# Kernel optimization log

Measured on AMD Instinct MI355X. Metric: run time of the kernel, lower is better.

## Reference

```python
import jax, jax.numpy as jnp
import numpy as np

D_MODEL = 1024
HEADS = 16
D_FF = 2048
EPS = 1e-6


def _ln(z, alpha, beta):
    # Faithful to the repo's (buggy-looking) LayerNorm:
    # mu = z - mean; sigma = std + eps; out = (z - mu/sigma)*alpha + beta
    mean = jnp.mean(z, axis=-1, keepdims=True)
    std = jnp.std(z, axis=-1, keepdims=True, ddof=1)  # torch.std is unbiased
    return (z - (z - mean) / (std + EPS)) * alpha + beta


def setup_inputs() -> dict:
    key = jax.random.key(0)
    ks = jax.random.split(key, 16)
    B, S, D = 8, 1024, D_MODEL
    s = 0.02
    inp = {
        "x": jax.random.normal(ks[0], (B, S, D), dtype=jnp.float32),
        "mask": jax.random.randint(ks[1], (B, S), 0, 2, dtype=jnp.int32),
        "Wq": jax.random.normal(ks[2], (D, D), dtype=jnp.float32) * s,
        "bq": jnp.zeros((D,), dtype=jnp.float32),
        "Wk": jax.random.normal(ks[3], (D, D), dtype=jnp.float32) * s,
        "bk": jnp.zeros((D,), dtype=jnp.float32),
        "Wv": jax.random.normal(ks[4], (D, D), dtype=jnp.float32) * s,
        "bv": jnp.zeros((D,), dtype=jnp.float32),
        "Wo": jax.random.normal(ks[5], (D, D), dtype=jnp.float32) * s,
        "bo": jnp.zeros((D,), dtype=jnp.float32),
        "W1": jax.random.normal(ks[6], (D_FF, D), dtype=jnp.float32) * s,
        "b1": jnp.zeros((D_FF,), dtype=jnp.float32),
        "W2": jax.random.normal(ks[7], (D, D_FF), dtype=jnp.float32) * s,
        "b2": jnp.zeros((D,), dtype=jnp.float32),
        "alpha1": jnp.ones((D,), dtype=jnp.float32),
        "beta1": jnp.zeros((D,), dtype=jnp.float32),
        "alpha2": jnp.ones((D,), dtype=jnp.float32),
        "beta2": jnp.zeros((D,), dtype=jnp.float32),
    }
    return inp


def reference(x, mask, Wq, bq, Wk, bk, Wv, bv, Wo, bo, W1, b1, W2, b2,
              alpha1, beta1, alpha2, beta2):
    B, S, D = x.shape
    H, dk = HEADS, D // HEADS
    # QKV projections (torch Linear: y = x @ W.T + b), split heads -> [B,H,S,dk]
    Q = (x @ Wq.T + bq).reshape(B, S, H, dk).transpose(0, 2, 1, 3)
    K = (x @ Wk.T + bk).reshape(B, S, H, dk).transpose(0, 2, 1, 3)
    V = (x @ Wv.T + bv).reshape(B, S, H, dk).transpose(0, 2, 1, 3)
    scores = jnp.einsum('bhqd,bhkd->bhqk', Q, K) / jnp.sqrt(jnp.float32(dk))
    # faithful mask broadcast: [B,1,S,1] over query rows
    m = mask[:, None, :, None]
    scores = jnp.where(m == 0, jnp.float32(-1e9), scores)
    A = jax.nn.softmax(scores, axis=-1)
    O = jnp.einsum('bhqk,bhkd->bhqd', A, V).transpose(0, 2, 1, 3).reshape(B, S, D)
    attn_out = O @ Wo.T + bo
    x1 = _ln(x + attn_out, alpha1, beta1)
    h = jax.nn.relu(x1 @ W1.T + b1)
    ff = h @ W2.T + b2
    return _ln(x1 + ff, alpha2, beta2)
```

## Files before the change

### kernel.cpp

```cpp
#include <hip/hip_runtime.h>
#include <cstdint>
#include <cstddef>

#define D_MODEL 1024
#define HEADS   16
#define DKH     64
#define D_FF    2048
#define SEQ     1024
#define BATCH   8
#define MROWS   (BATCH*SEQ)
#define LN_EPS  1e-6f

typedef __bf16 bh8 __attribute__((ext_vector_type(8)));
typedef float  f32x4 __attribute__((ext_vector_type(4)));
typedef unsigned short us8 __attribute__((ext_vector_type(8)));

__device__ __forceinline__ unsigned short f2bf(float f) {
  union { float f; unsigned int u; } c; c.f = f;
  unsigned int u = c.u;
  u = u + 0x7fffu + ((u >> 16) & 1u);
  return (unsigned short)(u >> 16);
}

__device__ __forceinline__ bh8 as_bh8(us8 v) { return __builtin_bit_cast(bh8, v); }

__device__ __forceinline__ void gl16(const unsigned short* g, unsigned short* l) {
  __builtin_amdgcn_global_load_lds(
      (const __attribute__((address_space(1))) unsigned int*)g,
      (__attribute__((address_space(3))) unsigned int*)l, 16, 0, 0);
}

__global__ void cast_bf16_k(const float* __restrict__ in, unsigned short* __restrict__ out, int n4) {
  int i = blockIdx.x * blockDim.x + threadIdx.x;
  if (i < n4) {
    float4 v = ((const float4*)in)[i];
    ushort4 o;
    o.x = f2bf(v.x); o.y = f2bf(v.y); o.z = f2bf(v.z); o.w = f2bf(v.w);
    ((ushort4*)out)[i] = o;
  }
}

__global__ void castw_k(const float* __restrict__ wq, const float* __restrict__ wk,
                        const float* __restrict__ wv, const float* __restrict__ wo,
                        const float* __restrict__ w1, const float* __restrict__ w2,
                        unsigned short* __restrict__ oqkv, unsigned short* __restrict__ oo,
                        unsigned short* __restrict__ o1, unsigned short* __restrict__ o2) {
  int i = blockIdx.x * blockDim.x + threadIdx.x;
  const int seg = i >> 18;
  const int loc = i & 262143;
  const float* src; unsigned short* dst; int il, ol;
  if (seg < 3)      { src = (seg == 0) ? wq : (seg == 1) ? wk : wv; dst = oqkv; il = loc; ol = seg * 262144 + loc; }
  else if (seg == 3){ src = wo; dst = oo; il = loc; ol = loc; }
  else if (seg < 6) { src = w1; dst = o1; il = (seg - 4) * 262144 + loc; ol = il; }
  else              { src = w2; dst = o2; il = (seg - 6) * 262144 + loc; ol = il; }
  float4 v = ((const float4*)src)[il];
  ushort4 o;
  o.x = f2bf(v.x); o.y = f2bf(v.y); o.z = f2bf(v.z); o.w = f2bf(v.w);
  ((ushort4*)dst)[ol] = o;
}

#define BM 128
#define BN 128
#define BK 64

template<int EPI>
__global__ __launch_bounds__(256)
void gemm_bt(const unsigned short* __restrict__ A, const unsigned short* __restrict__ Bw,
             const float* __restrict__ b0, const float* __restrict__ b1f,
             const float* __restrict__ b2f, const float* __restrict__ resid,
             void* __restrict__ out0, void* __restrict__ out1, void* __restrict__ out2,
             int M, int N, int K)
{
  __shared__ __align__(16) unsigned short As[BM * BK];
  __shared__ __align__(16) unsigned short Bs[BN * BK];

  const int tid  = threadIdx.x;
  const int lane = tid & 63;
  const int w    = tid >> 6;
  const int wr   = w >> 1;
  const int wc   = w & 1;
  const int l15  = lane & 15;
  const int l4   = lane >> 4;

  const int brow = blockIdx.y * BM;
  const int bcol = blockIdx.x * BN;

  int rowj[4], offj[4];
  #pragma unroll
  for (int j = 0; j < 4; ++j) {
    const int c = tid + j * 256;
    rowj[j] = c >> 3;
    offj[j] = ((c & 7) ^ ((c >> 3) & 7)) * 8;
  }

  const unsigned short* Ag = A  + (size_t)brow * K;
  const unsigned short* Bg = Bw + (size_t)bcol * K;

  f32x4 acc[4][4] = {};
  const int sw7 = l15 & 7;

  for (int k0 = 0; k0 < K; k0 += BK) {
    #pragma unroll
    for (int j = 0; j < 4; ++j)
      gl16(Ag + (size_t)rowj[j] * K + k0 + offj[j], &As[(tid + j * 256) * 8]);
    #pragma unroll
    for (int j = 0; j < 4; ++j)
      gl16(Bg + (size_t)rowj[j] * K + k0 + offj[j], &Bs[(tid + j * 256) * 8]);
    __syncthreads();

    #pragma unroll
    for (int h = 0; h < 2; ++h) {
      const int slot = ((h * 4 + l4) ^ sw7) * 8;
      us8 aF[4], bF[4];
      #pragma unroll
      for (int mi = 0; mi < 4; ++mi)
        aF[mi] = *(const us8*)(&As[(wr * 64 + mi * 16 + l15) * BK + slot]);
      #pragma unroll
      for (int ni = 0; ni < 4; ++ni)
        bF[ni] = *(const us8*)(&Bs[(wc * 64 + ni * 16 + l15) * BK + slot]);
      #pragma unroll
      for (int mi = 0; mi < 4; ++mi)
        #pragma unroll
        for (int ni = 0; ni < 4; ++ni)
          acc[mi][ni] = __builtin_amdgcn_mfma_f32_16x16x32_bf16(
              as_bh8(aF[mi]), as_bh8(bF[ni]), acc[mi][ni], 0, 0, 0);
    }
    __syncthreads();
  }

  const int tt = bcol >> 10;
  #pragma unroll
  for (int mi = 0; mi < 4; ++mi) {
    #pragma unroll
    for (int ni = 0; ni < 4; ++ni) {
      const int gcol = bcol + wc * 64 + ni * 16 + l15;
      if (EPI == 4) {
        const int ccol = gcol & 1023;
        const float bv = ((tt == 0) ? b0 : (tt == 1) ? b1f : b2f)[ccol];
        const int grow0 = brow + wr * 64 + mi * 16 + l4 * 4;
        if (tt == 2) {
          const int bb = grow0 >> 10;
          const int s0 = grow0 & 1023;
          ushort4 pk;
          pk.x = f2bf(acc[mi][ni][0] + bv);
          pk.y = f2bf(acc[mi][ni][1] + bv);
          pk.z = f2bf(acc[mi][ni][2] + bv);
          pk.w = f2bf(acc[mi][ni][3] + bv);
          *(ushort4*)((unsigned short*)out2 + ((size_t)bb * D_MODEL + ccol) * SEQ + s0) = pk;
        } else {
          unsigned short* ob = (unsigned short*)(tt == 0 ? out0 : out1);
          #pragma unroll
          for (int v = 0; v < 4; ++v)
            ob[(size_t)(grow0 + v) * D_MODEL + ccol] = f2bf(acc[mi][ni][v] + bv);
        }
      } else {
        const float bv = b0[gcol];
        #pragma unroll
        for (int v = 0; v < 4; ++v) {
          const int grow = brow + wr * 64 + mi * 16 + l4 * 4 + v;
          float val = acc[mi][ni][v] + bv;
          if (EPI == 3) val = fmaxf(val, 0.0f);
          if (EPI == 2) {
            val += resid[(size_t)grow * N + gcol];
            ((float*)out0)[(size_t)grow * N + gcol] = val;
          } else {
            ((unsigned short*)out0)[(size_t)grow * N + gcol] = f2bf(val);
          }
        }
      }
    }
  }
}

__global__ __launch_bounds__(256)
void attn_k(const unsigned short* __restrict__ Q, const unsigned short* __restrict__ Kb,
            const unsigned short* __restrict__ Vt, const int* __restrict__ mask,
            unsigned short* __restrict__ O)
{
  __shared__ __align__(16) unsigned short Ks[2][64][64];
  __shared__ __align__(16) unsigned short Vs[2][64][64];
  __shared__ __align__(16) unsigned short Pl[4][16][88];

  const int bid = blockIdx.x;
  const int qc = bid & 15;
  const int h  = (bid >> 4) & 15;
  const int b  = bid >> 8;
  const int q0 = qc * 64;

  const int tid  = threadIdx.x;
  const int lane = tid & 63;
  const int w    = tid >> 6;
  const int l15  = lane & 15;
  const int l4   = lane >> 4;

  const int c0 = tid, c1 = tid + 256;
  const int kr0 = c0 >> 3, ke0 = ((c0 & 7) ^ (kr0 & 7)) * 8;
  const int kr1 = c1 >> 3, ke1 = ((c1 & 7) ^ (kr1 & 7)) * 8;

  const unsigned short* Kbase = Kb + ((size_t)b * SEQ) * D_MODEL + h * DKH;
  const unsigned short* Vbase = Vt + ((size_t)b * D_MODEL + h * DKH) * SEQ;

  const unsigned short* qp = Q + ((size_t)(b * SEQ + q0 + w * 16 + l15)) * D_MODEL + h * DKH + l4 * 8;
  const bh8 aQ0 = as_bh8(*(const us8*)qp);
  const bh8 aQ1 = as_bh8(*(const us8*)(qp + 32));

  float msel[4];
  #pragma unroll
  for (int v = 0; v < 4; ++v)
    msel[v] = mask[b * SEQ + q0 + w * 16 + l4 * 4 + v] ? 0.125f : 0.0f;

  float l[4] = {0.f, 0.f, 0.f, 0.f};
  f32x4 oacc[4] = {};

  gl16(Kbase + (size_t)kr0 * D_MODEL + ke0, &Ks[0][0][0] + c0 * 8);
  gl16(Kbase + (size_t)kr1 * D_MODEL + ke1, &Ks[0][0][0] + c1 * 8);
  gl16(Vbase + (size_t)kr0 * SEQ + ke0,     &Vs[0][0][0] + c0 * 8);
  gl16(Vbase + (size_t)kr1 * SEQ + ke1,     &Vs[0][0][0] + c1 * 8);
  __syncthreads();

  for (int t = 0; t < 16; ++t) {
    const int cur = t & 1;
    if (t < 15) {
      const int kv = (t + 1) * 64;
      gl16(Kbase + (size_t)(kv + kr0) * D_MODEL + ke0, &Ks[cur ^ 1][0][0] + c0 * 8);
      gl16(Kbase + (size_t)(kv + kr1) * D_MODEL + ke1, &Ks[cur ^ 1][0][0] + c1 * 8);
      gl16(Vbase + (size_t)kr0 * SEQ + kv + ke0,       &Vs[cur ^ 1][0][0] + c0 * 8);
      gl16(Vbase + (size_t)kr1 * SEQ + kv + ke1,       &Vs[cur ^ 1][0][0] + c1 * 8);
    }

    f32x4 s[4];
    #pragma unroll
    for (int kt = 0; kt < 4; ++kt) {
      const int row = kt * 16 + l15;
      const int swz = l15 & 7;
      bh8 bK0 = as_bh8(*(const us8*)(&Ks[cur][row][(l4 ^ swz) * 8]));
      bh8 bK1 = as_bh8(*(const us8*)(&Ks[cur][row][((4 + l4) ^ swz) * 8]));
      f32x4 t0 = {0.f, 0.f, 0.f, 0.f};
      t0 = __builtin_amdgcn_mfma_f32_16x16x32_bf16(aQ0, bK0, t0, 0, 0, 0);
      t0 = __builtin_amdgcn_mfma_f32_16x16x32_bf16(aQ1, bK1, t0, 0, 0, 0);
      s[kt] = t0;
    }

    #pragma unroll
    for (int v = 0; v < 4; ++v) {
      float ls = 0.f;
      #pragma unroll
      for (int kt = 0; kt < 4; ++kt) {
        float e = __expf(s[kt][v] * msel[v]);
        s[kt][v] = e;
        ls += e;
      }
      l[v] += ls;
    }

    #pragma unroll
    for (int kt = 0; kt < 4; ++kt)
      #pragma unroll
      for (int v = 0; v < 4; ++v)
        Pl[w][l4 * 4 + v][kt * 16 + l15] = f2bf(s[kt][v]);

    #pragma unroll
    for (int ks = 0; ks < 2; ++ks) {
      bh8 aP = as_bh8(*(const us8*)(&Pl[w][l15][ks * 32 + l4 * 8]));
      #pragma unroll
      for (int ds = 0; ds < 4; ++ds) {
        const int row = ds * 16 + l15;
        bh8 bV = as_bh8(*(const us8*)(&Vs[cur][row][((ks * 4 + l4) ^ (l15 & 7)) * 8]));
        oacc[ds] = __builtin_amdgcn_mfma_f32_16x16x32_bf16(aP, bV, oacc[ds], 0, 0, 0);
      }
    }
    __syncthreads();
  }

  #pragma unroll
  for (int v = 0; v < 4; ++v) {
    float lv = l[v];
    #pragma unroll
    for (int d = 1; d < 16; d <<= 1) lv += __shfl_xor(lv, d, 64);
    const float inv = 1.0f / lv;
    const int q = q0 + w * 16 + l4 * 4 + v;
    #pragma unroll
    for (int ds = 0; ds < 4; ++ds)
      O[((size_t)(b * SEQ + q)) * D_MODEL + h * DKH + ds * 16 + l15] =
          f2bf(oacc[ds][v] * inv);
  }
}

template<bool WBF>
__global__ __launch_bounds__(256)
void ln_k(const float* __restrict__ z, const float* __restrict__ alpha,
          const float* __restrict__ beta, float* __restrict__ yf,
          unsigned short* __restrict__ yb)
{
  const int row = blockIdx.x;
  const int tid = threadIdx.x;
  const float4 v = ((const float4*)(z + (size_t)row * D_MODEL))[tid];
  float s  = v.x + v.y + v.z + v.w;
  float ss = v.x * v.x + v.y * v.y + v.z * v.z + v.w * v.w;
  #pragma unroll
  for (int d = 1; d < 64; d <<= 1) {
    s  += __shfl_xor(s, d, 64);
    ss += __shfl_xor(ss, d, 64);
  }
  __shared__ float red[8];
  const int w = tid >> 6;
  if ((tid & 63) == 0) { red[w * 2] = s; red[w * 2 + 1] = ss; }
  __syncthreads();
  const float S  = red[0] + red[2] + red[4] + red[6];
  const float SS = red[1] + red[3] + red[5] + red[7];
  const float mean = S * (1.0f / 1024.0f);
  float var = (SS - 1024.0f * mean * mean) * (1.0f / 1023.0f);
  var = fmaxf(var, 0.0f);
  const float invd = 1.0f / (sqrtf(var) + LN_EPS);

  const float4 a  = ((const float4*)alpha)[tid];
  const float4 be = ((const float4*)beta)[tid];
  float4 y;
  y.x = (v.x - (v.x - mean) * invd) * a.x + be.x;
  y.y = (v.y - (v.y - mean) * invd) * a.y + be.y;
  y.z = (v.z - (v.z - mean) * invd) * a.z + be.z;
  y.w = (v.w - (v.w - mean) * invd) * a.w + be.w;
  ((float4*)(yf + (size_t)row * D_MODEL))[tid] = y;
  if (WBF) {
    ushort4 pk;
    pk.x = f2bf(y.x); pk.y = f2bf(y.y); pk.z = f2bf(y.z); pk.w = f2bf(y.w);
    ((ushort4*)(yb + (size_t)row * D_MODEL))[tid] = pk;
  }
}

extern "C" void kernel_launch(void* const* d_in, const int* in_sizes, int n_in,
                              void* d_out, int out_size, void* d_ws, size_t ws_size,
                              hipStream_t stream) {
  const float* x    = (const float*)d_in[0];
  const int*   mask = (const int*)d_in[1];
  const float* Wq = (const float*)d_in[2];  const float* bq = (const float*)d_in[3];
  const float* Wk = (const float*)d_in[4];  const float* bk = (const float*)d_in[5];
  const float* Wv = (const float*)d_in[6];  const float* bv = (const float*)d_in[7];
  const float* Wo = (const float*)d_in[8];  const float* bo = (const float*)d_in[9];
  const float* W1 = (const float*)d_in[10]; const float* b1 = (const float*)d_in[11];
  const float* W2 = (const float*)d_in[12]; const float* b2 = (const float*)d_in[13];
  const float* alpha1 = (const float*)d_in[14]; const float* beta1 = (const float*)d_in[15];
  const float* alpha2 = (const float*)d_in[16]; const float* beta2 = (const float*)d_in[17];
  (void)in_sizes; (void)n_in; (void)out_size; (void)ws_size;

  char* ws = (char*)d_ws;
  const size_t MB = (size_t)1 << 20;
  unsigned short* xb    = (unsigned short*)(ws + 0 * MB);
  unsigned short* Wqkvb = (unsigned short*)(ws + 16 * MB);
  unsigned short* Wob   = (unsigned short*)(ws + 22 * MB);
  unsigned short* W1b   = (unsigned short*)(ws + 24 * MB);
  unsigned short* W2b   = (unsigned short*)(ws + 28 * MB);
  unsigned short* Qb    = (unsigned short*)(ws + 32 * MB);
  unsigned short* Kb2   = (unsigned short*)(ws + 48 * MB);
  unsigned short* Vt    = (unsigned short*)(ws + 64 * MB);
  unsigned short* Ob    = (unsigned short*)(ws + 80 * MB);
  float*          zf    = (float*)(ws + 96 * MB);
  float*          x1f   = (float*)(ws + 128 * MB);
  unsigned short* x1b   = (unsigned short*)(ws + 160 * MB);
  unsigned short* hb    = Qb;

  cast_bf16_k<<<8192, 256, 0, stream>>>(x, xb, MROWS * D_MODEL / 4);
  castw_k<<<8192, 256, 0, stream>>>(Wq, Wk, Wv, Wo, W1, W2, Wqkvb, Wob, W1b, W2b);

  gemm_bt<4><<<dim3(24, 64), 256, 0, stream>>>(xb, Wqkvb, bq, bk, bv, nullptr,
                                               Qb, Kb2, Vt, MROWS, 3072, D_MODEL);

  attn_k<<<BATCH * HEADS * (SEQ / 64), 256, 0, stream>>>(Qb, Kb2, Vt, mask, Ob);

  gemm_bt<2><<<dim3(8, 64), 256, 0, stream>>>(Ob, Wob, bo, nullptr, nullptr, x,
                                              zf, nullptr, nullptr, MROWS, D_MODEL, D_MODEL);
  ln_k<true><<<MROWS, 256, 0, stream>>>(zf, alpha1, beta1, x1f, x1b);

  gemm_bt<3><<<dim3(16, 64), 256, 0, stream>>>(x1b, W1b, b1, nullptr, nullptr, nullptr,
                                               hb, nullptr, nullptr, MROWS, D_FF, D_MODEL);
  gemm_bt<2><<<dim3(8, 64), 256, 0, stream>>>(hb, W2b, b2, nullptr, nullptr, x1f,
                                              zf, nullptr, nullptr, MROWS, D_MODEL, D_FF);

  ln_k<false><<<MROWS, 256, 0, stream>>>(zf, alpha2, beta2, (float*)d_out, nullptr);
}
```

Baseline: 319.2 us.

## Double-buffer GEMM LDS tiles, swizzle block order, prescale Q for exp2

The GEMM now keeps two LDS buffers and prefetches two K-tiles ahead, using explicit vmcnt and lgkmcnt waits with raw barriers, so global loads overlap the MFMA work. Fragments are loaded to registers before the next stage is issued. Blocks are remapped in both GEMM and attention so that neighbouring workgroups are spread across groups of eight, which targets cache locality. Attention folds the mask and the 1/sqrt(dk)*log2(e) scale into Q once, so the inner loop is a bare exp2; this adds bf16 rounding of the scaled Q and doubles GEMM LDS use, which may lower occupancy.

```diff
diff --git a/kernel.cpp b/kernel.cpp
--- a/kernel.cpp
+++ b/kernel.cpp
@@ -20,6 +20,10 @@
   unsigned int u = c.u;
   u = u + 0x7fffu + ((u >> 16) & 1u);
   return (unsigned short)(u >> 16);
+}
+__device__ __forceinline__ float bf2f(unsigned short h) {
+  union { unsigned int u; float f; } c; c.u = ((unsigned int)h) << 16;
+  return c.f;
 }
 
 __device__ __forceinline__ bh8 as_bh8(us8 v) { return __builtin_bit_cast(bh8, v); }
@@ -71,8 +75,8 @@
              void* __restrict__ out0, void* __restrict__ out1, void* __restrict__ out2,
              int M, int N, int K)
 {
-  __shared__ __align__(16) unsigned short As[BM * BK];
-  __shared__ __align__(16) unsigned short Bs[BN * BK];
+  __shared__ __align__(16) unsigned short As[2][BM * BK];
+  __shared__ __align__(16) unsigned short Bs[2][BM * BK];
 
   const int tid  = threadIdx.x;
   const int lane = tid & 63;
@@ -82,8 +86,12 @@
   const int l15  = lane & 15;
   const int l4   = lane >> 4;
 
-  const int brow = blockIdx.y * BM;
-  const int bcol = blockIdx.x * BN;
+  const int gx  = gridDim.x;
+  const int nwg = gx * gridDim.y;
+  int lin = blockIdx.y * gx + blockIdx.x;
+  lin = (lin & 7) * (nwg >> 3) + (lin >> 3);
+  const int brow = (lin / gx) * BM;
+  const int bcol = (lin % gx) * BN;
 
   int rowj[4], offj[4];
   #pragma unroll
@@ -96,36 +104,52 @@
   const unsigned short* Ag = A  + (size_t)brow * K;
   const unsigned short* Bg = Bw + (size_t)bcol * K;
 
+  auto stage = [&](int bsel, int k0) {
+    #pragma unroll
+    for (int j = 0; j < 4; ++j)
+      gl16(Ag + (size_t)rowj[j] * K + k0 + offj[j], &As[bsel][(tid + j * 256) * 8]);
+    #pragma unroll
+    for (int j = 0; j < 4; ++j)
+      gl16(Bg + (size_t)rowj[j] * K + k0 + offj[j], &Bs[bsel][(tid + j * 256) * 8]);
+  };
+
+  const int NT = K / BK;
+  stage(0, 0);
+  stage(1, BK);
+
   f32x4 acc[4][4] = {};
   const int sw7 = l15 & 7;
 
-  for (int k0 = 0; k0 < K; k0 += BK) {
-    #pragma unroll
-    for (int j = 0; j < 4; ++j)
-      gl16(Ag + (size_t)rowj[j] * K + k0 + offj[j], &As[(tid + j * 256) * 8]);
-    #pragma unroll
-    for (int j = 0; j < 4; ++j)
-      gl16(Bg + (size_t)rowj[j] * K + k0 + offj[j], &Bs[(tid + j * 256) * 8]);
-    __syncthreads();
-
+  for (int t = 0; t < NT; ++t) {
+    const int cur = t & 1;
+    if (t + 1 < NT) { asm volatile("s_waitcnt vmcnt(8)" ::: "memory"); }
+    else            { asm volatile("s_waitcnt vmcnt(0)" ::: "memory"); }
+    __builtin_amdgcn_s_barrier();
+
+    us8 aF[2][4], bF[2][4];
     #pragma unroll
     for (int h = 0; h < 2; ++h) {
       const int slot = ((h * 4 + l4) ^ sw7) * 8;
-      us8 aF[4], bF[4];
       #pragma unroll
       for (int mi = 0; mi < 4; ++mi)
-        aF[mi] = *(const us8*)(&As[(wr * 64 + mi * 16 + l15) * BK + slot]);
+        aF[h][mi] = *(const us8*)(&As[cur][(wr * 64 + mi * 16 + l15) * BK + slot]);
       #pragma unroll
       for (int ni = 0; ni < 4; ++ni)
-        bF[ni] = *(const us8*)(&Bs[(wc * 64 + ni * 16 + l15) * BK + slot]);
+        bF[h][ni] = *(const us8*)(&Bs[cur][(wc * 64 + ni * 16 + l15) * BK + slot]);
+    }
+    asm volatile("s_waitcnt lgkmcnt(0)" ::: "memory");
+    __builtin_amdgcn_s_barrier();
+
+    if (t + 2 < NT) stage(cur, (t + 2) * BK);
+
+    #pragma unroll
+    for (int h = 0; h < 2; ++h)
       #pragma unroll
       for (int mi = 0; mi < 4; ++mi)
         #pragma unroll
         for (int ni = 0; ni < 4; ++ni)
           acc[mi][ni] = __builtin_amdgcn_mfma_f32_16x16x32_bf16(
-              as_bh8(aF[mi]), as_bh8(bF[ni]), acc[mi][ni], 0, 0, 0);
-    }
-    __syncthreads();
+              as_bh8(aF[h][mi]), as_bh8(bF[h][ni]), acc[mi][ni], 0, 0, 0);
   }
 
   const int tt = bcol >> 10;
@@ -181,7 +205,7 @@
   __shared__ __align__(16) unsigned short Vs[2][64][64];
   __shared__ __align__(16) unsigned short Pl[4][16][88];
 
-  const int bid = blockIdx.x;
+  const int bid = (blockIdx.x & 7) * 256 + (blockIdx.x >> 3);
   const int qc = bid & 15;
   const int h  = (bid >> 4) & 15;
   const int b  = bid >> 8;
@@ -201,13 +225,17 @@
   const unsigned short* Vbase = Vt + ((size_t)b * D_MODEL + h * DKH) * SEQ;
 
   const unsigned short* qp = Q + ((size_t)(b * SEQ + q0 + w * 16 + l15)) * D_MODEL + h * DKH + l4 * 8;
-  const bh8 aQ0 = as_bh8(*(const us8*)qp);
-  const bh8 aQ1 = as_bh8(*(const us8*)(qp + 32));
-
-  float msel[4];
+  const float qs = mask[b * SEQ + q0 + w * 16 + l15] ? 0.18033688011112042f : 0.0f;
+  us8 q0r = *(const us8*)qp;
+  us8 q1r = *(const us8*)(qp + 32);
+  us8 q0s, q1s;
   #pragma unroll
-  for (int v = 0; v < 4; ++v)
-    msel[v] = mask[b * SEQ + q0 + w * 16 + l4 * 4 + v] ? 0.125f : 0.0f;
+  for (int j = 0; j < 8; ++j) {
+    q0s[j] = f2bf(bf2f(q0r[j]) * qs);
+    q1s[j] = f2bf(bf2f(q1r[j]) * qs);
+  }
+  const bh8 aQ0 = as_bh8(q0s);
+  const bh8 aQ1 = as_bh8(q1s);
 
   float l[4] = {0.f, 0.f, 0.f, 0.f};
   f32x4 oacc[4] = {};
@@ -246,7 +274,7 @@
       float ls = 0.f;
       #pragma unroll
       for (int kt = 0; kt < 4; ++kt) {
-        float e = __expf(s[kt][v] * msel[v]);
+        float e = exp2f(s[kt][v]);
         s[kt][v] = e;
         ls += e;
       }
```

After: 307.8 us. 1.04x faster.
